# Optimization experiments

Hardware: AMD Instinct MI355X
Metric: run time of the kernel (lower is better)

## Reference

```python
import jax, jax.numpy as jnp
import numpy as np

BETA = 1.0  # write blending coefficient (beta in original module)


def ste(x):
    # Binarize with straight-through estimator: forward (x>0.5), backward identity.
    b = (x > 0.5).astype(x.dtype)
    return x + jax.lax.stop_gradient(b - x)


def setup_inputs() -> dict:
    key = jax.random.key(0)
    k0, k1, k2 = jax.random.split(key, 3)
    B, H, W, HID = 8, 512, 512, 64
    f0 = jax.random.uniform(k0, (B, 1, H, W), dtype=jnp.float32)
    W1 = jax.random.normal(k1, (9, HID), dtype=jnp.float32) * (1.0 / np.sqrt(9.0))
    b1 = jnp.zeros((HID,), dtype=jnp.float32)
    W2 = jax.random.normal(k2, (HID, 1), dtype=jnp.float32) * (1.0 / np.sqrt(HID))
    b2 = jnp.zeros((1,), dtype=jnp.float32)
    return {"f0": f0, "W1": W1, "b1": b1, "W2": W2, "b2": b2, "T": 16}


def reference(f0, W1, b1, W2, b2, T):
    B, _, H, Wd = f0.shape

    def step(f, _):
        f_read = ste(f)                                            # (B,1,H,W) binarized read
        pad = jnp.pad(f_read, ((0, 0), (0, 0), (1, 1), (1, 1)), mode="wrap")
        # 3x3 neighborhoods, row-major top-left -> bottom-right: (B,H,W,9)
        neigh = jnp.stack(
            [pad[:, 0, i:i + H, j:j + Wd] for i in range(3) for j in range(3)],
            axis=-1,
        )
        h = jax.nn.relu(jnp.einsum("bhwn,nk->bhwk", neigh, W1) + b1)
        logits = (jnp.einsum("bhwk,ko->bhwo", h, W2) + b2)[..., 0]  # (B,H,W)
        w_bits = ste(jax.nn.sigmoid(logits))[:, None]               # (B,1,H,W)
        f_new = (1.0 - BETA) * f + BETA * w_bits
        return f_new, f_new

    _, rest = jax.lax.scan(step, f0, None, length=T - 1)
    fields = jnp.concatenate([f0[None], rest], axis=0)  # (T,B,1,H,W)
    return fields
```

## Files before the change

kernel.cpp:

```cpp
#include <hip/hip_runtime.h>

#define HH 512
#define WW 512
#define WPR 16
#define RO 16
#define HALO 15
#define ROWS (RO + 2 * HALO)
#define OW 8
#define TW 10

#define STEP_BARRIER() do {                                   \
    asm volatile("s_waitcnt lgkmcnt(0)" ::: "memory");        \
    __builtin_amdgcn_s_barrier();                             \
    __builtin_amdgcn_sched_barrier(0);                        \
} while (0)

__global__ __launch_bounds__(256) void init_field(const float* __restrict__ f0,
                                                  float* __restrict__ out,
                                                  unsigned long long* __restrict__ field) {
    int c = blockIdx.x * 256 + threadIdx.x;
    float v = f0[c];
    out[c] = v;
    unsigned long long m = __ballot(v > 0.5f);
    if ((threadIdx.x & 63) == 0) field[c >> 6] = m;
}

__global__ __launch_bounds__(512) void mega(const unsigned int* __restrict__ field,
                                            const float* __restrict__ W1,
                                            const float* __restrict__ b1,
                                            const float* __restrict__ W2,
                                            const float* __restrict__ b2,
                                            int hid, float* __restrict__ out,
                                            int n, int T) {
    __shared__ unsigned int rule[512];
    __shared__ unsigned int lutp[256];
    __shared__ unsigned int bufA[ROWS * TW];
    __shared__ unsigned int bufB[ROWS * TW];

    const int tid = threadIdx.x;
    const int cg = blockIdx.x & 1;
    const int rg = (blockIdx.x >> 1) & 31;
    const int b  = blockIdx.x >> 6;
    const int r0 = rg * RO;
    const int q0 = cg * OW;
    const int c0 = cg * (OW * 32);

    {
        int p = tid;
        float logit = b2[0];
        for (int k = 0; k < hid; ++k) {
            float a = b1[k];
#pragma unroll
            for (int nn = 0; nn < 9; ++nn)
                if (p & (1 << nn)) a += W1[nn * hid + k];
            logit += fmaxf(a, 0.0f) * W2[k];
        }
        rule[p] = (logit > 0.0f) ? 1u : 0u;
    }
    __syncthreads();

    if (tid < 256) {
        unsigned int wv = 0;
#pragma unroll
        for (int k = 0; k < 16; ++k) {
            unsigned int e = (unsigned int)tid * 16u + k;
            unsigned int u = e & 15u, m = (e >> 4) & 15u, d = (e >> 8) & 15u;
            unsigned int i0 = (u & 7u) | ((m & 7u) << 3) | ((d & 7u) << 6);
            unsigned int i1 = (u >> 1) | ((m >> 1) << 3) | ((d >> 1) << 6);
            wv |= (rule[i0] | (rule[i1] << 1)) << (2 * k);
        }
        lutp[tid] = wv;
    }

    {
        const unsigned int* F = field + b * (HH * WPR);
        for (int i = tid; i < ROWS * TW; i += 512) {
            int l = i / TW, tw = i - l * TW;
            int g  = (r0 - HALO + l) & (HH - 1);
            int gw = (q0 - 1 + tw) & (WPR - 1);
            bufA[i] = F[g * WPR + gw];
        }
    }
    __syncthreads();

    unsigned int* oldb = bufA;
    unsigned int* newb = bufB;
    float* outb = out + (size_t)b * (HH * WW);

    for (int t = 1; t < T; ++t) {
        const int hi = ROWS - t;
        const int lq = tid / TW;
        const int w  = tid - lq * TW;
        const int l  = t + lq;
        if (l < hi) {
            const unsigned int* Ru = oldb + (l - 1) * TW;
            const unsigned int* Rm = oldb + l * TW;
            const unsigned int* Rd = oldb + (l + 1) * TW;
            const int wl = (w == 0) ? 0 : w - 1;
            const int wn = (w == TW - 1) ? TW - 1 : w + 1;
            unsigned long long eu = ((((unsigned long long)Ru[wn] << 32) | Ru[w]) << 1) | (Ru[wl] >> 31);
            unsigned long long em = ((((unsigned long long)Rm[wn] << 32) | Rm[w]) << 1) | (Rm[wl] >> 31);
            unsigned long long ed = ((((unsigned long long)Rd[wn] << 32) | Rd[w]) << 1) | (Rd[wl] >> 31);
            unsigned int ow = 0;
#pragma unroll
            for (int j = 0; j < 16; ++j) {
                unsigned int idx = (unsigned int)((eu >> (2 * j)) & 15ull)
                                 | ((unsigned int)((em >> (2 * j)) & 15ull) << 4)
                                 | ((unsigned int)((ed >> (2 * j)) & 15ull) << 8);
                ow |= ((lutp[idx >> 4] >> ((idx & 15u) * 2)) & 3u) << (2 * j);
            }
            newb[l * TW + w] = ow;
        }
        STEP_BARRIER();

        float* outt = outb + (size_t)t * n;
#pragma unroll
        for (int rep = 0; rep < 2; ++rep) {
            int cell = (rep * 512 + tid) * 4;
            int lr  = cell >> 8;
            int col = cell & 255;
            unsigned int wv = newb[(HALO + lr) * TW + 1 + (col >> 5)];
            unsigned int nib = (wv >> (col & 31)) & 15u;
            float4 v;
            v.x = (float)(nib & 1u);
            v.y = (float)((nib >> 1) & 1u);
            v.z = (float)((nib >> 2) & 1u);
            v.w = (float)(nib >> 3);
            *(float4*)(outt + (size_t)(r0 + lr) * WW + c0 + col) = v;
        }
        unsigned int* tmp = oldb; oldb = newb; newb = tmp;
    }
}

extern "C" void kernel_launch(void* const* d_in, const int* in_sizes, int n_in,
                              void* d_out, int out_size, void* d_ws, size_t ws_size,
                              hipStream_t stream) {
    const float* f0 = (const float*)d_in[0];
    const float* W1 = (const float*)d_in[1];
    const float* b1 = (const float*)d_in[2];
    const float* W2 = (const float*)d_in[3];
    const float* b2 = (const float*)d_in[4];
    float* out = (float*)d_out;

    const int n = in_sizes[0];
    const int hid = in_sizes[2];
    const int T = out_size / n;
    const int B = n / (HH * WW);

    unsigned long long* fld = (unsigned long long*)d_ws;

    init_field<<<n / 256, 256, 0, stream>>>(f0, out, fld);
    mega<<<B * (HH / RO) * 2, 512, 0, stream>>>((const unsigned int*)fld,
                                                W1, b1, W2, b2, hid, out, n, T);
}
```

Before: 66.51 us.

## Hoist rule LUT build into init kernel and halve rows per block

The 512-entry MLP rule table and packed LUT are now computed once by block 0 of the init kernel and written to workspace, instead of being rebuilt in every mega block. Each mega block now owns 8 output rows instead of 16, doubling the grid to 1024 blocks and halving the per-step output writes per thread. The cost is more redundant halo computation, since a 15-row halo on each side now surrounds only 8 output rows. Block 0 of the init kernel also carries the serial MLP evaluation.

Result: faster. 63.36 us (-4.7%).

```diff
diff --git a/kernel.cpp b/kernel.cpp
--- a/kernel.cpp
+++ b/kernel.cpp
@@ -3,7 +3,7 @@
 #define HH 512
 #define WW 512
 #define WPR 16
-#define RO 16
+#define RO 8
 #define HALO 15
 #define ROWS (RO + 2 * HALO)
 #define OW 8
@@ -15,63 +15,69 @@
     __builtin_amdgcn_sched_barrier(0);                        \
 } while (0)
 
-__global__ __launch_bounds__(256) void init_field(const float* __restrict__ f0,
-                                                  float* __restrict__ out,
-                                                  unsigned long long* __restrict__ field) {
-    int c = blockIdx.x * 256 + threadIdx.x;
+__global__ __launch_bounds__(512) void init_pack(const float* __restrict__ f0,
+                                                 const float* __restrict__ W1,
+                                                 const float* __restrict__ b1,
+                                                 const float* __restrict__ W2,
+                                                 const float* __restrict__ b2,
+                                                 int hid,
+                                                 float* __restrict__ out,
+                                                 unsigned long long* __restrict__ field,
+                                                 unsigned int* __restrict__ lutg) {
+    __shared__ unsigned int rule[512];
+    const int tid = threadIdx.x;
+    int c = blockIdx.x * 512 + tid;
     float v = f0[c];
     out[c] = v;
     unsigned long long m = __ballot(v > 0.5f);
-    if ((threadIdx.x & 63) == 0) field[c >> 6] = m;
+    if ((tid & 63) == 0) field[c >> 6] = m;
+
+    if (blockIdx.x == 0) {
+        {
+            int p = tid;
+            float logit = b2[0];
+            for (int k = 0; k < hid; ++k) {
+                float a = b1[k];
+#pragma unroll
+                for (int nn = 0; nn < 9; ++nn)
+                    if (p & (1 << nn)) a += W1[nn * hid + k];
+                logit += fmaxf(a, 0.0f) * W2[k];
+            }
+            rule[p] = (logit > 0.0f) ? 1u : 0u;
+        }
+        __syncthreads();
+        if (tid < 256) {
+            unsigned int wv = 0;
+#pragma unroll
+            for (int k = 0; k < 16; ++k) {
+                unsigned int e = (unsigned int)tid * 16u + k;
+                unsigned int u = e & 15u, mm = (e >> 4) & 15u, d = (e >> 8) & 15u;
+                unsigned int i0 = (u & 7u) | ((mm & 7u) << 3) | ((d & 7u) << 6);
+                unsigned int i1 = (u >> 1) | ((mm >> 1) << 3) | ((d >> 1) << 6);
+                wv |= (rule[i0] | (rule[i1] << 1)) << (2 * k);
+            }
+            lutg[tid] = wv;
+        }
+    }
 }
 
 __global__ __launch_bounds__(512) void mega(const unsigned int* __restrict__ field,
-                                            const float* __restrict__ W1,
-                                            const float* __restrict__ b1,
-                                            const float* __restrict__ W2,
-                                            const float* __restrict__ b2,
-                                            int hid, float* __restrict__ out,
+                                            const unsigned int* __restrict__ lutg,
+                                            float* __restrict__ out,
                                             int n, int T) {
-    __shared__ unsigned int rule[512];
     __shared__ unsigned int lutp[256];
     __shared__ unsigned int bufA[ROWS * TW];
     __shared__ unsigned int bufB[ROWS * TW];
 
     const int tid = threadIdx.x;
     const int cg = blockIdx.x & 1;
-    const int rg = (blockIdx.x >> 1) & 31;
-    const int b  = blockIdx.x >> 6;
+    const int rg = (blockIdx.x >> 1) & 63;
+    const int b  = blockIdx.x >> 7;
     const int r0 = rg * RO;
     const int q0 = cg * OW;
     const int c0 = cg * (OW * 32);
 
-    {
-        int p = tid;
-        float logit = b2[0];
-        for (int k = 0; k < hid; ++k) {
-            float a = b1[k];
-#pragma unroll
-            for (int nn = 0; nn < 9; ++nn)
-                if (p & (1 << nn)) a += W1[nn * hid + k];
-            logit += fmaxf(a, 0.0f) * W2[k];
-        }
-        rule[p] = (logit > 0.0f) ? 1u : 0u;
-    }
-    __syncthreads();
-
-    if (tid < 256) {
-        unsigned int wv = 0;
-#pragma unroll
-        for (int k = 0; k < 16; ++k) {
-            unsigned int e = (unsigned int)tid * 16u + k;
-            unsigned int u = e & 15u, m = (e >> 4) & 15u, d = (e >> 8) & 15u;
-            unsigned int i0 = (u & 7u) | ((m & 7u) << 3) | ((d & 7u) << 6);
-            unsigned int i1 = (u >> 1) | ((m >> 1) << 3) | ((d >> 1) << 6);
-            wv |= (rule[i0] | (rule[i1] << 1)) << (2 * k);
-        }
-        lutp[tid] = wv;
-    }
-
+    if (tid < 256) lutp[tid] = lutg[tid];
     {
         const unsigned int* F = field + b * (HH * WPR);
         for (int i = tid; i < ROWS * TW; i += 512) {
@@ -114,9 +120,8 @@
         STEP_BARRIER();
 
         float* outt = outb + (size_t)t * n;
-#pragma unroll
-        for (int rep = 0; rep < 2; ++rep) {
-            int cell = (rep * 512 + tid) * 4;
+        {
+            int cell = tid * 4;
             int lr  = cell >> 8;
             int col = cell & 255;
             unsigned int wv = newb[(HALO + lr) * TW + 1 + (col >> 5)];
@@ -147,9 +152,11 @@
     const int T = out_size / n;
     const int B = n / (HH * WW);
 
-    unsigned long long* fld = (unsigned long long*)d_ws;
+    char* ws = (char*)d_ws;
+    unsigned int* lutg = (unsigned int*)ws;
+    unsigned long long* fld = (unsigned long long*)(ws + 1024);
 
-    init_field<<<n / 256, 256, 0, stream>>>(f0, out, fld);
-    mega<<<B * (HH / RO) * 2, 512, 0, stream>>>((const unsigned int*)fld,
-                                                W1, b1, W2, b2, hid, out, n, T);
+    init_pack<<<n / 512, 512, 0, stream>>>(f0, W1, b1, W2, b2, hid, out, fld, lutg);
+    mega<<<B * (HH / RO) * 2, 512, 0, stream>>>((const unsigned int*)fld, lutg,
+                                                out, n, T);
 }
```

## Split bit-packed evolution from float expansion and fuse init into evolve kernel

Applied to the files above, without the earlier changes.

Folds binarization of f0 into the evolution kernel, which now covers full-width rows per block with wrap-around columns instead of two column halves. The evolution kernel writes packed bit frames to workspace, and a separate expand kernel turns them into float outputs across the whole GPU. The aim is to take the large float stores off the 256-block serial evolution loop and spread them over many blocks, at the cost of an extra kernel launch and a bit-frame round trip through memory. T and batch size are now hardcoded (15 steps, 8 batches, 256 blocks) rather than derived from the sizes.

Result: slower. 80.54 us (+21.1%).

```diff
diff --git a/kernel.cpp b/kernel.cpp
--- a/kernel.cpp
+++ b/kernel.cpp
@@ -6,8 +6,7 @@
 #define RO 16
 #define HALO 15
 #define ROWS (RO + 2 * HALO)
-#define OW 8
-#define TW 10
+#define FRAME_WORDS (8 * HH * WPR)
 
 #define STEP_BARRIER() do {                                   \
     asm volatile("s_waitcnt lgkmcnt(0)" ::: "memory");        \
@@ -15,37 +14,25 @@
     __builtin_amdgcn_sched_barrier(0);                        \
 } while (0)
 
-__global__ __launch_bounds__(256) void init_field(const float* __restrict__ f0,
-                                                  float* __restrict__ out,
-                                                  unsigned long long* __restrict__ field) {
-    int c = blockIdx.x * 256 + threadIdx.x;
-    float v = f0[c];
-    out[c] = v;
-    unsigned long long m = __ballot(v > 0.5f);
-    if ((threadIdx.x & 63) == 0) field[c >> 6] = m;
-}
-
-__global__ __launch_bounds__(512) void mega(const unsigned int* __restrict__ field,
-                                            const float* __restrict__ W1,
-                                            const float* __restrict__ b1,
-                                            const float* __restrict__ W2,
-                                            const float* __restrict__ b2,
-                                            int hid, float* __restrict__ out,
-                                            int n, int T) {
+__global__ __launch_bounds__(768) void evolve(const float* __restrict__ f0,
+                                              const float* __restrict__ W1,
+                                              const float* __restrict__ b1,
+                                              const float* __restrict__ W2,
+                                              const float* __restrict__ b2,
+                                              int hid,
+                                              float* __restrict__ out,
+                                              unsigned int* __restrict__ fields) {
     __shared__ unsigned int rule[512];
     __shared__ unsigned int lutp[256];
-    __shared__ unsigned int bufA[ROWS * TW];
-    __shared__ unsigned int bufB[ROWS * TW];
+    __shared__ unsigned int bufA[ROWS * WPR];
+    __shared__ unsigned int bufB[ROWS * WPR];
 
     const int tid = threadIdx.x;
-    const int cg = blockIdx.x & 1;
-    const int rg = (blockIdx.x >> 1) & 31;
-    const int b  = blockIdx.x >> 6;
+    const int rg = blockIdx.x & 31;
+    const int b  = blockIdx.x >> 5;
     const int r0 = rg * RO;
-    const int q0 = cg * OW;
-    const int c0 = cg * (OW * 32);
 
-    {
+    if (tid < 512) {
         int p = tid;
         float logit = b2[0];
         for (int k = 0; k < hid; ++k) {
@@ -64,40 +51,43 @@
 #pragma unroll
         for (int k = 0; k < 16; ++k) {
             unsigned int e = (unsigned int)tid * 16u + k;
-            unsigned int u = e & 15u, m = (e >> 4) & 15u, d = (e >> 8) & 15u;
-            unsigned int i0 = (u & 7u) | ((m & 7u) << 3) | ((d & 7u) << 6);
-            unsigned int i1 = (u >> 1) | ((m >> 1) << 3) | ((d >> 1) << 6);
+            unsigned int u = e & 15u, mm = (e >> 4) & 15u, d = (e >> 8) & 15u;
+            unsigned int i0 = (u & 7u) | ((mm & 7u) << 3) | ((d & 7u) << 6);
+            unsigned int i1 = (u >> 1) | ((mm >> 1) << 3) | ((d >> 1) << 6);
             wv |= (rule[i0] | (rule[i1] << 1)) << (2 * k);
         }
         lutp[tid] = wv;
     }
 
     {
-        const unsigned int* F = field + b * (HH * WPR);
-        for (int i = tid; i < ROWS * TW; i += 512) {
-            int l = i / TW, tw = i - l * TW;
-            int g  = (r0 - HALO + l) & (HH - 1);
-            int gw = (q0 - 1 + tw) & (WPR - 1);
-            bufA[i] = F[g * WPR + gw];
+        const float* f0b = f0 + (size_t)b * (HH * WW);
+        float* out0 = out + (size_t)b * (HH * WW);
+        const int lane = tid & 63;
+        for (int i = tid; i < ROWS * WW; i += 768) {
+            int l = i >> 9, c = i & 511;
+            int gr = (r0 - HALO + l) & (HH - 1);
+            float v = f0b[(size_t)gr * WW + c];
+            unsigned long long m = __ballot(v > 0.5f);
+            if (lane == 0)  bufA[l * WPR + (c >> 5)] = (unsigned int)m;
+            if (lane == 32) bufA[l * WPR + (c >> 5)] = (unsigned int)(m >> 32);
+            if (l >= HALO && l < HALO + RO)
+                out0[(size_t)gr * WW + c] = v;
         }
     }
     __syncthreads();
 
     unsigned int* oldb = bufA;
     unsigned int* newb = bufB;
-    float* outb = out + (size_t)b * (HH * WW);
 
-    for (int t = 1; t < T; ++t) {
-        const int hi = ROWS - t;
-        const int lq = tid / TW;
-        const int w  = tid - lq * TW;
-        const int l  = t + lq;
-        if (l < hi) {
-            const unsigned int* Ru = oldb + (l - 1) * TW;
-            const unsigned int* Rm = oldb + l * TW;
-            const unsigned int* Rd = oldb + (l + 1) * TW;
-            const int wl = (w == 0) ? 0 : w - 1;
-            const int wn = (w == TW - 1) ? TW - 1 : w + 1;
+    for (int s = 1; s <= HALO; ++s) {
+        const int lq = tid >> 4;
+        const int w  = tid & 15;
+        const int l  = s + lq;
+        if (l < ROWS - s) {
+            const unsigned int* Ru = oldb + (l - 1) * WPR;
+            const unsigned int* Rm = oldb + l * WPR;
+            const unsigned int* Rd = oldb + (l + 1) * WPR;
+            const int wl = (w + 15) & 15, wn = (w + 1) & 15;
             unsigned long long eu = ((((unsigned long long)Ru[wn] << 32) | Ru[w]) << 1) | (Ru[wl] >> 31);
             unsigned long long em = ((((unsigned long long)Rm[wn] << 32) | Rm[w]) << 1) | (Rm[wl] >> 31);
             unsigned long long ed = ((((unsigned long long)Rd[wn] << 32) | Rd[w]) << 1) | (Rd[wl] >> 31);
@@ -109,27 +99,31 @@
                                  | ((unsigned int)((ed >> (2 * j)) & 15ull) << 8);
                 ow |= ((lutp[idx >> 4] >> ((idx & 15u) * 2)) & 3u) << (2 * j);
             }
-            newb[l * TW + w] = ow;
+            newb[l * WPR + w] = ow;
         }
         STEP_BARRIER();
 
-        float* outt = outb + (size_t)t * n;
-#pragma unroll
-        for (int rep = 0; rep < 2; ++rep) {
-            int cell = (rep * 512 + tid) * 4;
-            int lr  = cell >> 8;
-            int col = cell & 255;
-            unsigned int wv = newb[(HALO + lr) * TW + 1 + (col >> 5)];
-            unsigned int nib = (wv >> (col & 31)) & 15u;
-            float4 v;
-            v.x = (float)(nib & 1u);
-            v.y = (float)((nib >> 1) & 1u);
-            v.z = (float)((nib >> 2) & 1u);
-            v.w = (float)(nib >> 3);
-            *(float4*)(outt + (size_t)(r0 + lr) * WW + c0 + col) = v;
+        if (tid < RO * WPR) {
+            int lr = tid >> 4, w2 = tid & 15;
+            fields[(size_t)(s - 1) * FRAME_WORDS + b * (HH * WPR)
+                   + (size_t)(r0 + lr) * WPR + w2] = newb[(HALO + lr) * WPR + w2];
         }
         unsigned int* tmp = oldb; oldb = newb; newb = tmp;
     }
+}
+
+__global__ __launch_bounds__(512) void expand(const unsigned int* __restrict__ fields,
+                                              float* __restrict__ out, int n) {
+    const int f  = blockIdx.x >> 10;
+    const int g4 = ((blockIdx.x & 1023) << 9) + threadIdx.x;
+    unsigned int wv = fields[(size_t)f * FRAME_WORDS + (g4 >> 3)];
+    unsigned int nib = (wv >> ((g4 & 7) * 4)) & 15u;
+    float4 v;
+    v.x = (float)(nib & 1u);
+    v.y = (float)((nib >> 1) & 1u);
+    v.z = (float)((nib >> 2) & 1u);
+    v.w = (float)(nib >> 3);
+    ((float4*)out)[(size_t)(f + 1) * (n >> 2) + g4] = v;
 }
 
 extern "C" void kernel_launch(void* const* d_in, const int* in_sizes, int n_in,
@@ -144,12 +138,9 @@
 
     const int n = in_sizes[0];
     const int hid = in_sizes[2];
-    const int T = out_size / n;
-    const int B = n / (HH * WW);
 
-    unsigned long long* fld = (unsigned long long*)d_ws;
+    unsigned int* fields = (unsigned int*)d_ws;
 
-    init_field<<<n / 256, 256, 0, stream>>>(f0, out, fld);
-    mega<<<B * (HH / RO) * 2, 512, 0, stream>>>((const unsigned int*)fld,
-                                                W1, b1, W2, b2, hid, out, n, T);
+    evolve<<<256, 768, 0, stream>>>(f0, W1, b1, W2, b2, hid, out, fields);
+    expand<<<15 * 1024, 512, 0, stream>>>(fields, out, n);
 }
```
